# Performance work log

Hardware: AMD Instinct MI355X
Metric: run time of the kernel (lower is better)

Reference implementation:

```python
import jax, jax.numpy as jnp
import numpy as np

IN_FEATURES = 1024
OUT_FEATURES = 64
DEGREE = 3
NUM_KNOTS = 10
BATCH = 8192
K0 = NUM_KNOTS + DEGREE  # number of basis columns / control points per edge


def b_spline_basis(x, knots, degree):
    """Vectorized Cox-de Boor recursion.
    x: (..., ) values in [0,1]; knots: (K0+1,).
    Returns (..., K0) basis; last `degree` columns are zero-padded (matches
    control_points width of num_knots+degree as in the original module).
    """
    t = knots
    n0 = t.shape[0] - 1  # = K0 degree-0 intervals
    xe = x[..., None]
    basis = ((xe >= t[:-1]) & (xe < t[1:])).astype(x.dtype)  # (..., K0)
    for p in range(1, degree + 1):
        ti = t[: n0 - p]
        tip = t[p:n0]
        ti1 = t[1 : n0 - p + 1]
        tip1 = t[p + 1 : n0 + 1]
        d1 = jnp.where(tip - ti > 0, tip - ti, jnp.ones_like(ti))
        d2 = jnp.where(tip1 - ti1 > 0, tip1 - ti1, jnp.ones_like(ti1))
        left = jnp.where(tip - ti > 0, (xe - ti) / d1, 0.0) * basis[..., : n0 - p]
        right = jnp.where(tip1 - ti1 > 0, (tip1 - xe) / d2, 0.0) * basis[..., 1 : n0 - p + 1]
        new = left + right
        pad = jnp.zeros(x.shape + (p,), x.dtype)
        basis = jnp.concatenate([new, pad], axis=-1)
    return basis


def setup_inputs() -> dict:
    key = jax.random.key(0)
    k1, k2 = jax.random.split(key)
    x = jax.random.uniform(k1, (BATCH, IN_FEATURES), dtype=jnp.float32)
    knots = jnp.linspace(0.0, 1.0, NUM_KNOTS + DEGREE + 1, dtype=jnp.float32)
    control_points = jax.random.normal(k2, (OUT_FEATURES, IN_FEATURES, K0), dtype=jnp.float32)
    return {"x": x, "knots": knots, "control_points": control_points}


def reference(x, knots, control_points):
    # basis: (B, in, K0) computed once per input feature (original recomputes
    # it out_features times inside a double loop -- same math, fused here).
    basis = b_spline_basis(x, knots, DEGREE)
    # outputs[b, o] = sum_j sum_k basis[b, j, k] * control_points[o, j, k]
    return jnp.einsum("bjk,ojk->bo", basis, control_points)
```

## Files before the change

kernel.cpp:

```cpp
#include <hip/hip_runtime.h>
#include <hip/hip_bf16.h>
#include <stdint.h>

#define IN_F   1024
#define OUT_F  64
#define BATCH  8192
#define BM     256
#define NTHR   256
#define JSPLIT 32
#define JPB    (IN_F / JSPLIT)
#define JC     4
#define NCH    (JPB / JC)
#define BT_B   (JC * 2048)
#define X_B    (BM * JC * 4)
#define BUF_B  (BT_B + X_B)
#define TBL_B  (14 * 32 * 48)
#define LDS_T  (TBL_B + 2 * BUF_B)
#define OUTSZ  (BATCH * OUT_F)

typedef __attribute__((ext_vector_type(8)))  short short8;
typedef __attribute__((ext_vector_type(16))) float f32x16;

__device__ __forceinline__ void gll16(const void* g, void* l) {
    __builtin_amdgcn_global_load_lds(
        (const __attribute__((address_space(1))) uint32_t*)g,
        (__attribute__((address_space(3))) uint32_t*)l,
        16, 0, 0);
}

__global__ void kan_prep(const float* __restrict__ cp, __hip_bfloat16* __restrict__ bt) {
    int j = blockIdx.x * 4 + (threadIdx.x >> 6);
    int o = threadIdx.x & 63;
    const float* src = cp + ((size_t)o * IN_F + j) * 13;
    float v[16];
#pragma unroll
    for (int k = 0; k < 10; ++k) v[k] = src[k];
#pragma unroll
    for (int k = 10; k < 16; ++k) v[k] = 0.0f;
    __hip_bfloat16* dst = bt + (size_t)j * 1024;
#pragma unroll
    for (int kh = 0; kh < 2; ++kh)
#pragma unroll
        for (int e = 0; e < 8; ++e)
            dst[kh * 512 + o * 8 + e] = __float2bfloat16(v[kh * 8 + e]);
}

template<bool PART>
__launch_bounds__(NTHR, 3)
__global__ void kan_main(const float* __restrict__ x,
                         const __hip_bfloat16* __restrict__ bt,
                         void* __restrict__ outp) {
    __shared__ __attribute__((aligned(16))) char lds[LDS_T];

    const int tid   = threadIdx.x;
    const int w     = tid >> 6;
    const int lane  = tid & 63;
    const int l31   = lane & 31;
    const int khalf = lane >> 5;

    const int r0 = blockIdx.x * BM;
    const int j0 = blockIdx.y * JPB;

    for (int e = tid; e < 14 * 32; e += NTHR) {
        const int m = e >> 5, u5 = e & 31;
        const float uu = (u5 + 0.5f) * (1.0f / 32.0f);
        const float u2 = uu * uu;
        const float omu = 1.0f - uu;
        const float o2 = omu * omu;
        const float B3 = u2 * (uu * (1.0f / 6.0f));
        const float B0 = o2 * (omu * (1.0f / 6.0f));
        const float B1 = __builtin_fmaf(u2, __builtin_fmaf(uu, 0.5f, -1.0f), 2.0f / 3.0f);
        const float B2 = 1.0f - B0 - B1 - B3;
        uint32_t P01, P23;
        asm("v_cvt_pk_bf16_f32 %0, %1, %2" : "=v"(P01) : "v"(B0), "v"(B1));
        asm("v_cvt_pk_bf16_f32 %0, %1, %2" : "=v"(P23) : "v"(B2), "v"(B3));
        const uint64_t V = ((uint64_t)P23 << 32) | (uint64_t)P01;
#pragma unroll
        for (int h = 0; h < 2; ++h) {
            const int c0 = 48 + (h << 7);
            const int p = (m << 4) - c0;
            const uint64_t sl = V << ((uint32_t)p & 63);
            const uint64_t sr = V >> ((uint32_t)(-p) & 63);
            const uint64_t t0 = (p < 0) ? sr : sl;
            const uint64_t q0 = ((uint32_t)(p + 63) < 127u) ? t0 : 0ull;
            const uint64_t t1 = (p < 64) ? sr : sl;
            const uint64_t q1 = ((uint32_t)(p - 16) < 112u) ? t1 : 0ull;
            uint64_t* d = (uint64_t*)(lds + e * 48 + h * 16);
            d[0] = q0; d[1] = q1;
        }
    }

    const char* btg = (const char*)bt + (size_t)j0 * 2048 + (size_t)tid * 16;
    const char* xgt = (const char*)(x + (size_t)(r0 + tid) * IN_F + j0);
    const int   wofs = w << 10;

#define STAGE(ch, bi) do {                                        \
        char* base_ = lds + TBL_B + (bi) * BUF_B;                 \
        const char* gb_ = btg + (size_t)(ch) * BT_B;              \
        gll16(gb_,        base_ + wofs);                          \
        gll16(gb_ + 4096, base_ + 4096 + wofs);                   \
        gll16(xgt + (ch) * (JC * 4), base_ + BT_B + wofs);        \
    } while (0)

#define AFRAG(xv) ({                                              \
        const float t416_ = (xv) * 416.0f;           \
        const int i_ = (int)t416_;                 \
        const int s_ = ((i_ << 1) + i_) << 4;         \
        *(const short8*)(lds + s_ + (khalf << 4)); })

#define COMPUTE(bi) do {                                                      \
        const char* base = lds + TBL_B + (bi) * BUF_B;                        \
        float xa0[4], xa1[4];                                                 \
        const char* xr = base + BT_B + (((w << 6) + l31) << 4);               \
        *(float4*)xa0 = *(const float4*)(xr);              \
        *(float4*)xa1 = *(const float4*)(xr + 512);     \
        const char* bbb = base + (khalf << 10) + l31 * 16;                    \
        _Pragma("unroll")                                                     \
        for (int jl = 0; jl < JC; ++jl) {                                     \
            const short8 b0 = *(const short8*)(bbb + jl * 2048);              \
            const short8 b1 = *(const short8*)(bbb + jl * 2048 + 512);        \
            const short8 a0 = AFRAG(xa0[jl]);                                 \
            const short8 a1 = AFRAG(xa1[jl]);                                 \
            acc00 = __builtin_amdgcn_mfma_f32_32x32x16_bf16(a0, b0, acc00, 0, 0, 0); \
            acc01 = __builtin_amdgcn_mfma_f32_32x32x16_bf16(a0, b1, acc01, 0, 0, 0); \
            acc10 = __builtin_amdgcn_mfma_f32_32x32x16_bf16(a1, b0, acc10, 0, 0, 0); \
            acc11 = __builtin_amdgcn_mfma_f32_32x32x16_bf16(a1, b1, acc11, 0, 0, 0); \
        }                                                                     \
    } while (0)

    f32x16 acc00, acc01, acc10, acc11;
#pragma unroll
    for (int i = 0; i < 16; ++i) {
        acc00[i] = 0.0f; acc01[i] = 0.0f; acc10[i] = 0.0f; acc11[i] = 0.0f;
    }

    STAGE(0, 0);
    STAGE(1, 1);
    __syncthreads();

    int cur = 0;
#pragma unroll 1
    for (int ch = 0; ch < NCH; ++ch) {
        if (ch >= 2) {
            asm volatile("s_waitcnt vmcnt(3)" ::: "memory");
            __builtin_amdgcn_s_barrier();
            __builtin_amdgcn_sched_barrier(0);
        }
        COMPUTE(cur);
        if (ch + 2 < NCH) {
            __builtin_amdgcn_s_barrier();
            __builtin_amdgcn_sched_barrier(0);
            STAGE(ch + 2, cur);
        }
        cur ^= 1;
    }
#undef STAGE
#undef AFRAG
#undef COMPUTE

    if (PART) {
        __hip_bfloat16* op = (__hip_bfloat16*)outp + (size_t)blockIdx.y * OUTSZ;
#pragma unroll
        for (int r = 0; r < 16; ++r) {
            const int crow = (r & 3) + 8 * (r >> 2) + 4 * khalf;
            __hip_bfloat16* p0 = op + (size_t)(r0 + (w << 6) + crow) * OUT_F;
            __hip_bfloat16* p1 = p0 + 32 * OUT_F;
            p0[l31]      = __float2bfloat16(acc00[r]);
            p0[l31 + 32] = __float2bfloat16(acc01[r]);
            p1[l31]      = __float2bfloat16(acc10[r]);
            p1[l31 + 32] = __float2bfloat16(acc11[r]);
        }
    } else {
        float* op = (float*)outp;
#pragma unroll
        for (int r = 0; r < 16; ++r) {
            const int crow = (r & 3) + 8 * (r >> 2) + 4 * khalf;
            float* p0 = op + (size_t)(r0 + (w << 6) + crow) * OUT_F;
            float* p1 = p0 + 32 * OUT_F;
            atomicAdd(p0 + l31,      acc00[r]);
            atomicAdd(p0 + l31 + 32, acc01[r]);
            atomicAdd(p1 + l31,      acc10[r]);
            atomicAdd(p1 + l31 + 32, acc11[r]);
        }
    }
}

__global__ void kan_reduce(const __hip_bfloat16* __restrict__ part,
                           float* __restrict__ out) {
    const int i = (blockIdx.x * 256 + threadIdx.x) * 8;
    float s[8] = {0, 0, 0, 0, 0, 0, 0, 0};
#pragma unroll
    for (int b = 0; b < JSPLIT; ++b) {
        const short8 v = *(const short8*)(part + (size_t)b * OUTSZ + i);
#pragma unroll
        for (int e = 0; e < 8; ++e) {
            union { uint32_t u; float f; } c;
            c.u = ((uint32_t)(uint16_t)v[e]) << 16;
            s[e] += c.f;
        }
    }
    float4 lo = {s[0], s[1], s[2], s[3]}, hi = {s[4], s[5], s[6], s[7]};
    *(float4*)(out + i)     = lo;
    *(float4*)(out + i + 4) = hi;
}

extern "C" void kernel_launch(void* const* d_in, const int* in_sizes, int n_in,
                              void* d_out, int out_size, void* d_ws, size_t ws_size,
                              hipStream_t stream) {
    const float* x  = (const float*)d_in[0];
    const float* cp = (const float*)d_in[2];
    float* out = (float*)d_out;
    __hip_bfloat16* bt   = (__hip_bfloat16*)d_ws;
    __hip_bfloat16* part = (__hip_bfloat16*)((char*)d_ws + 2u * 1024u * 1024u);

    const size_t need = 2u * 1024u * 1024u + (size_t)JSPLIT * OUTSZ * 2u;
    const bool use_part = ws_size >= need;

    kan_prep<<<dim3(IN_F / 4), dim3(256), 0, stream>>>(cp, bt);
    if (use_part) {
        kan_main<true><<<dim3(BATCH / BM, JSPLIT), dim3(NTHR), 0, stream>>>(x, bt, (void*)part);
        kan_reduce<<<dim3(OUTSZ / 2048), dim3(256), 0, stream>>>(part, out);
    } else {
        hipMemsetAsync(d_out, 0, (size_t)out_size * sizeof(float), stream);
        kan_main<false><<<dim3(BATCH / BM, JSPLIT), dim3(NTHR), 0, stream>>>(x, bt, (void*)d_out);
    }
}
```

Before: 43.29 us.

## Double row tile per block to 512 with four MFMA row fragments per wave

Each block now covers 512 batch rows instead of 256, so each wave keeps eight 32x32 accumulators and reuses every loaded B fragment across four A fragments. The first two stage loads are now issued before the basis lookup table is built, overlapping that setup with global loads, and the wait count and final drain are adjusted for four loads per stage. This halves grid blocks and B-tile traffic per row, at the cost of more registers, occupancy lowered to 2 blocks/SM, and a larger LDS footprint.

```diff
diff --git a/kernel.cpp b/kernel.cpp
--- a/kernel.cpp
+++ b/kernel.cpp
@@ -5,15 +5,15 @@
 #define IN_F   1024
 #define OUT_F  64
 #define BATCH  8192
-#define BM     256
+#define BM     512
 #define NTHR   256
 #define JSPLIT 32
 #define JPB    (IN_F / JSPLIT)
 #define JC     4
 #define NCH    (JPB / JC)
 #define BT_B   (JC * 2048)
-#define X_B    (BM * JC * 4)
-#define BUF_B  (BT_B + X_B)
+#define XC_B   (BM * JC * 4)
+#define BUF_B  (BT_B + XC_B)
 #define TBL_B  (14 * 32 * 48)
 #define LDS_T  (TBL_B + 2 * BUF_B)
 #define OUTSZ  (BATCH * OUT_F)
@@ -46,7 +46,7 @@
 }
 
 template<bool PART>
-__launch_bounds__(NTHR, 3)
+__launch_bounds__(NTHR, 2)
 __global__ void kan_main(const float* __restrict__ x,
                          const __hip_bfloat16* __restrict__ bt,
                          void* __restrict__ outp) {
@@ -60,6 +60,22 @@
 
     const int r0 = blockIdx.x * BM;
     const int j0 = blockIdx.y * JPB;
+
+    const char* btg  = (const char*)bt + (size_t)j0 * 2048 + (size_t)tid * 16;
+    const char* xgt  = (const char*)x + ((size_t)(r0 + tid) * IN_F + j0) * 4;
+    const char* xgt2 = xgt + (size_t)256 * IN_F * 4;
+    const int   wofs = w << 10;
+
+#define STAGE(ch, bi) do {                                        \
+        char* b_ = lds + TBL_B + (bi) * BUF_B;                    \
+        gll16(btg + (size_t)(ch) * BT_B,        b_ + wofs);       \
+        gll16(btg + (size_t)(ch) * BT_B + 4096, b_ + 4096 + wofs);\
+        gll16(xgt  + (ch) * 16, b_ + BT_B + wofs);                \
+        gll16(xgt2 + (ch) * 16, b_ + BT_B + 4096 + wofs);         \
+    } while (0)
+
+    STAGE(0, 0);
+    STAGE(1, 1);
 
     for (int e = tid; e < 14 * 32; e += NTHR) {
         const int m = e >> 5, u5 = e & 31;
@@ -90,18 +106,6 @@
         }
     }
 
-    const char* btg = (const char*)bt + (size_t)j0 * 2048 + (size_t)tid * 16;
-    const char* xgt = (const char*)(x + (size_t)(r0 + tid) * IN_F + j0);
-    const int   wofs = w << 10;
-
-#define STAGE(ch, bi) do {                                        \
-        char* base_ = lds + TBL_B + (bi) * BUF_B;                 \
-        const char* gb_ = btg + (size_t)(ch) * BT_B;              \
-        gll16(gb_,        base_ + wofs);                          \
-        gll16(gb_ + 4096, base_ + 4096 + wofs);                   \
-        gll16(xgt + (ch) * (JC * 4), base_ + BT_B + wofs);        \
-    } while (0)
-
 #define AFRAG(xv) ({                                              \
         const float t416_ = (xv) * 416.0f;           \
         const int i_ = (int)t416_;                 \
@@ -110,39 +114,47 @@
 
 #define COMPUTE(bi) do {                                                      \
         const char* base = lds + TBL_B + (bi) * BUF_B;                        \
-        float xa0[4], xa1[4];                                                 \
-        const char* xr = base + BT_B + (((w << 6) + l31) << 4);               \
-        *(float4*)xa0 = *(const float4*)(xr);              \
-        *(float4*)xa1 = *(const float4*)(xr + 512);     \
+        const char* xr = base + BT_B + (((w << 7) + l31) << 4);               \
+        float xv0[4], xv1[4], xv2[4], xv3[4];                                 \
+        *(float4*)xv0 = *(const float4*)(xr);              \
+        *(float4*)xv1 = *(const float4*)(xr + 512);             \
+        *(float4*)xv2 = *(const float4*)(xr + 1024);            \
+        *(float4*)xv3 = *(const float4*)(xr + 1536);            \
         const char* bbb = base + (khalf << 10) + l31 * 16;                    \
         _Pragma("unroll")                                                     \
         for (int jl = 0; jl < JC; ++jl) {                                     \
             const short8 b0 = *(const short8*)(bbb + jl * 2048);              \
             const short8 b1 = *(const short8*)(bbb + jl * 2048 + 512);        \
-            const short8 a0 = AFRAG(xa0[jl]);                                 \
-            const short8 a1 = AFRAG(xa1[jl]);                                 \
+            const short8 a0 = AFRAG(xv0[jl]);                                 \
+            const short8 a1 = AFRAG(xv1[jl]);                                 \
+            const short8 a2 = AFRAG(xv2[jl]);                                 \
+            const short8 a3 = AFRAG(xv3[jl]);                                 \
             acc00 = __builtin_amdgcn_mfma_f32_32x32x16_bf16(a0, b0, acc00, 0, 0, 0); \
             acc01 = __builtin_amdgcn_mfma_f32_32x32x16_bf16(a0, b1, acc01, 0, 0, 0); \
             acc10 = __builtin_amdgcn_mfma_f32_32x32x16_bf16(a1, b0, acc10, 0, 0, 0); \
             acc11 = __builtin_amdgcn_mfma_f32_32x32x16_bf16(a1, b1, acc11, 0, 0, 0); \
+            acc20 = __builtin_amdgcn_mfma_f32_32x32x16_bf16(a2, b0, acc20, 0, 0, 0); \
+            acc21 = __builtin_amdgcn_mfma_f32_32x32x16_bf16(a2, b1, acc21, 0, 0, 0); \
+            acc30 = __builtin_amdgcn_mfma_f32_32x32x16_bf16(a3, b0, acc30, 0, 0, 0); \
+            acc31 = __builtin_amdgcn_mfma_f32_32x32x16_bf16(a3, b1, acc31, 0, 0, 0); \
         }                                                                     \
     } while (0)
 
-    f32x16 acc00, acc01, acc10, acc11;
+    f32x16 acc00, acc01, acc10, acc11, acc20, acc21, acc30, acc31;
 #pragma unroll
     for (int i = 0; i < 16; ++i) {
         acc00[i] = 0.0f; acc01[i] = 0.0f; acc10[i] = 0.0f; acc11[i] = 0.0f;
-    }
-
-    STAGE(0, 0);
-    STAGE(1, 1);
+        acc20[i] = 0.0f; acc21[i] = 0.0f; acc30[i] = 0.0f; acc31[i] = 0.0f;
+    }
+
     __syncthreads();
 
     int cur = 0;
 #pragma unroll 1
     for (int ch = 0; ch < NCH; ++ch) {
         if (ch >= 2) {
-            asm volatile("s_waitcnt vmcnt(3)" ::: "memory");
+            if (ch == NCH - 1) asm volatile("s_waitcnt vmcnt(0)" ::: "memory");
+            else               asm volatile("s_waitcnt vmcnt(4)" ::: "memory");
             __builtin_amdgcn_s_barrier();
             __builtin_amdgcn_sched_barrier(0);
         }
@@ -163,24 +175,36 @@
 #pragma unroll
         for (int r = 0; r < 16; ++r) {
             const int crow = (r & 3) + 8 * (r >> 2) + 4 * khalf;
-            __hip_bfloat16* p0 = op + (size_t)(r0 + (w << 6) + crow) * OUT_F;
-            __hip_bfloat16* p1 = p0 + 32 * OUT_F;
+            __hip_bfloat16* p0 = op + (size_t)(r0 + (w << 7) + crow) * OUT_F;
             p0[l31]      = __float2bfloat16(acc00[r]);
             p0[l31 + 32] = __float2bfloat16(acc01[r]);
+            __hip_bfloat16* p1 = p0 + 32 * OUT_F;
             p1[l31]      = __float2bfloat16(acc10[r]);
             p1[l31 + 32] = __float2bfloat16(acc11[r]);
+            __hip_bfloat16* p2 = p0 + 64 * OUT_F;
+            p2[l31]      = __float2bfloat16(acc20[r]);
+            p2[l31 + 32] = __float2bfloat16(acc21[r]);
+            __hip_bfloat16* p3 = p0 + 96 * OUT_F;
+            p3[l31]      = __float2bfloat16(acc30[r]);
+            p3[l31 + 32] = __float2bfloat16(acc31[r]);
         }
     } else {
         float* op = (float*)outp;
 #pragma unroll
         for (int r = 0; r < 16; ++r) {
             const int crow = (r & 3) + 8 * (r >> 2) + 4 * khalf;
-            float* p0 = op + (size_t)(r0 + (w << 6) + crow) * OUT_F;
-            float* p1 = p0 + 32 * OUT_F;
+            float* p0 = op + (size_t)(r0 + (w << 7) + crow) * OUT_F;
             atomicAdd(p0 + l31,      acc00[r]);
             atomicAdd(p0 + l31 + 32, acc01[r]);
+            float* p1 = p0 + 32 * OUT_F;
             atomicAdd(p1 + l31,      acc10[r]);
             atomicAdd(p1 + l31 + 32, acc11[r]);
+            float* p2 = p0 + 64 * OUT_F;
+            atomicAdd(p2 + l31,      acc20[r]);
+            atomicAdd(p2 + l31 + 32, acc21[r]);
+            float* p3 = p0 + 96 * OUT_F;
+            atomicAdd(p3 + l31,      acc30[r]);
+            atomicAdd(p3 + l31 + 32, acc31[r]);
         }
     }
 }
```

New measurement: 45.86 us. 1.06x slower.
